# Kernel optimization log

Hardware: AMD Instinct MI355X
Metric: run time of the kernel (lower is better)

Reference implementation:

```python
import jax, jax.numpy as jnp
import numpy as np

N_LAYERS, H, D, DH = 4, 16, 1024, 64
V_FR, V_EN = 32000, 32000
L_FR, L_EN, B = 513, 512, 2


def _pos_enc(x):
    # x: [L, B, D]; pe[i,j] = sin(i/10000^(j/D)) if j even else cos(i/10000^((j-1)/D))
    L, _, D_ = x.shape
    pos = jnp.arange(L, dtype=jnp.float32)[:, None]
    j = jnp.arange(D_)
    ang = pos / jnp.power(10000.0, (j - (j % 2)).astype(jnp.float32) / D_)
    pe = jnp.where(j % 2 == 0, jnp.sin(ang), jnp.cos(ang))
    return x + pe[:, None, :]


def _ln(x, g, b):
    mu = jnp.mean(x, -1, keepdims=True)
    var = jnp.mean((x - mu) ** 2, -1, keepdims=True)
    return (x - mu) * jax.lax.rsqrt(var + 1e-5) * g + b


def _mha(q_in, k_in, v_in, w, bias, causal):
    # w: [3, H, D, dh], bias: [3, H, dh]
    dh = w.shape[-1]
    Q = jnp.einsum('bld,hde->bhle', q_in, w[0]) + bias[0][None, :, None, :]
    K = jnp.einsum('bmd,hde->bhme', k_in, w[1]) + bias[1][None, :, None, :]
    V = jnp.einsum('bmd,hde->bhme', v_in, w[2]) + bias[2][None, :, None, :]
    s = jnp.einsum('bhle,bhme->bhlm', Q, K) / jnp.sqrt(jnp.float32(dh))
    if causal:
        m = jnp.tril(jnp.ones((s.shape[-2], s.shape[-1]), bool))
        s = jnp.where(m, s, -jnp.inf)
    a = jax.nn.softmax(s, axis=-1)
    o = jnp.einsum('bhlm,bhme->bhle', a, V)
    b_, h_, l_, dh_ = o.shape
    return o.transpose(0, 2, 1, 3).reshape(b_, l_, h_ * dh_)


def setup_inputs() -> dict:
    key = jax.random.key(0)
    ks = jax.random.split(key, 24)
    s = 0.02
    rn = lambda k, shp: jax.random.normal(k, shp, jnp.float32) * s
    return {
        'fr': jax.random.randint(ks[0], (L_FR, B), 0, V_FR),
        'en': jax.random.randint(ks[1], (L_EN, B), 0, V_EN),
        'emb_fr': rn(ks[2], (V_FR, D)),
        'emb_en': rn(ks[3], (V_EN, D)),
        'enc_qkv_w': rn(ks[4], (N_LAYERS, 3, H, D, DH)),
        'enc_qkv_b': rn(ks[5], (N_LAYERS, 3, H, DH)),
        'enc_fc1_w': rn(ks[6], (N_LAYERS, D, D)),
        'enc_fc1_b': rn(ks[7], (N_LAYERS, D)),
        'enc_fc2_w': rn(ks[8], (N_LAYERS, D, D)),
        'enc_fc2_b': rn(ks[9], (N_LAYERS, D)),
        'enc_ln_g': jnp.ones((N_LAYERS, 2, D)) + rn(ks[10], (N_LAYERS, 2, D)),
        'enc_ln_b': rn(ks[11], (N_LAYERS, 2, D)),
        'dec_self_qkv_w': rn(ks[12], (N_LAYERS, 3, H, D, DH)),
        'dec_self_qkv_b': rn(ks[13], (N_LAYERS, 3, H, DH)),
        'dec_cross_qkv_w': rn(ks[14], (N_LAYERS, 3, H, D, DH)),
        'dec_cross_qkv_b': rn(ks[15], (N_LAYERS, 3, H, DH)),
        'dec_fc1_w': rn(ks[16], (N_LAYERS, D, D)),
        'dec_fc1_b': rn(ks[17], (N_LAYERS, D)),
        'dec_fc2_w': rn(ks[18], (N_LAYERS, D, D)),
        'dec_fc2_b': rn(ks[19], (N_LAYERS, D)),
        'dec_ln_g': jnp.ones((N_LAYERS, 3, D)) + rn(ks[20], (N_LAYERS, 3, D)),
        'dec_ln_b': rn(ks[21], (N_LAYERS, 3, D)),
        'out_w': rn(ks[22], (D, V_EN)),
        'out_b': rn(ks[23], (V_EN,)),
    }


def reference(fr, en, emb_fr, emb_en, enc_qkv_w, enc_qkv_b, enc_fc1_w, enc_fc1_b,
              enc_fc2_w, enc_fc2_b, enc_ln_g, enc_ln_b, dec_self_qkv_w,
              dec_self_qkv_b, dec_cross_qkv_w, dec_cross_qkv_b, dec_fc1_w,
              dec_fc1_b, dec_fc2_w, dec_fc2_b, dec_ln_g, dec_ln_b, out_w, out_b):
    # Encoder (dropout p=0 -> identity in eval math)
    x = _pos_enc(emb_fr[fr[1:]]).transpose(1, 0, 2)  # [B, L_src, D]
    for n in range(N_LAYERS):
        a = _mha(x, x, x, enc_qkv_w[n], enc_qkv_b[n], causal=False)
        x = _ln(x + a, enc_ln_g[n, 0], enc_ln_b[n, 0])
        h = jnp.maximum(x @ enc_fc1_w[n] + enc_fc1_b[n], 0.0) @ enc_fc2_w[n] + enc_fc2_b[n]
        x = _ln(x + h, enc_ln_g[n, 1], enc_ln_b[n, 1])
    enc_out = x
    # Decoder
    y = _pos_enc(emb_en[en]).transpose(1, 0, 2)  # [B, L_tgt, D]
    for n in range(N_LAYERS):
        a = _mha(y, y, y, dec_self_qkv_w[n], dec_self_qkv_b[n], causal=True)
        y = _ln(y + a, dec_ln_g[n, 0], dec_ln_b[n, 0])
        c = _mha(y, enc_out, enc_out, dec_cross_qkv_w[n], dec_cross_qkv_b[n], causal=False)
        y = _ln(y + c, dec_ln_g[n, 1], dec_ln_b[n, 1])
        h = jnp.maximum(y @ dec_fc1_w[n] + dec_fc1_b[n], 0.0) @ dec_fc2_w[n] + dec_fc2_b[n]
        y = _ln(y + h, dec_ln_g[n, 2], dec_ln_b[n, 2])
    return y @ out_w + out_b  # [B, L_tgt, V_EN]
```

## Files before the change

kernel.cpp:

```cpp
#include <hip/hip_runtime.h>
#include <stdint.h>
#include <stddef.h>

typedef unsigned short u16;
typedef __attribute__((ext_vector_type(8))) short bf16x8;
typedef __attribute__((ext_vector_type(4))) float f32x4;

#define DEV __device__ __forceinline__

DEV float b2f(u16 u) { union { float f; uint32_t i; } v; v.i = ((uint32_t)u) << 16; return v.f; }
DEV u16 f2b(float f) {
  uint32_t x = __float_as_uint(f);
  x += 0x7fffu + ((x >> 16) & 1u);
  return (u16)(x >> 16);
}
DEV bf16x8 ld8f(const float* f) {
  float4 a = *(const float4*)f;
  float4 b = *(const float4*)(f + 4);
  bf16x8 r;
  ((u16*)&r)[0] = f2b(a.x); ((u16*)&r)[1] = f2b(a.y);
  ((u16*)&r)[2] = f2b(a.z); ((u16*)&r)[3] = f2b(a.w);
  ((u16*)&r)[4] = f2b(b.x); ((u16*)&r)[5] = f2b(b.y);
  ((u16*)&r)[6] = f2b(b.z); ((u16*)&r)[7] = f2b(b.w);
  return r;
}
DEV void gload16(const u16* g, u16* l) {
  __builtin_amdgcn_global_load_lds((const __attribute__((address_space(1))) void*)g,
                                   (__attribute__((address_space(3))) void*)l, 16, 0, 0);
}
DEV f32x4 mfma16(bf16x8 a, bf16x8 b, f32x4 c) {
  return __builtin_amdgcn_mfma_f32_16x16x32_bf16(a, b, c, 0, 0, 0);
}

__global__ __launch_bounds__(256) void transpose_w(const float* __restrict__ src,
                                                   u16* __restrict__ dst, int K, int N) {
  __shared__ u16 t[32][33];
  int tx = threadIdx.x, ty = threadIdx.y;
  int k0 = blockIdx.x * 32, n0 = blockIdx.y * 32;
  size_t base = (size_t)blockIdx.z * K * N;
#pragma unroll
  for (int i = 0; i < 4; i++) {
    int k = ty + 8 * i;
    t[k][tx] = f2b(src[base + (size_t)(k0 + k) * N + n0 + tx]);
  }
  __syncthreads();
#pragma unroll
  for (int i = 0; i < 4; i++) {
    int n = ty + 8 * i;
    dst[base + (size_t)(n0 + n) * K + k0 + tx] = t[tx][n];
  }
}

__global__ __launch_bounds__(256) void embed_k(const int* __restrict__ tok, const float* __restrict__ emb,
                                               float* __restrict__ o32, u16* __restrict__ ob, int shift) {
  int row = blockIdx.x;
  int b = row >> 9, l = row & 511;
  int tk = tok[(size_t)(l + shift) * 2 + b];
  const float* e = emb + (size_t)tk * 1024;
  const float c0 = -9.210340371976184f / 1024.f;
#pragma unroll
  for (int i = 0; i < 4; i++) {
    int d = threadIdx.x + i * 256;
    int j2 = d & ~1;
    float ang = (float)l * expf(c0 * (float)j2);
    float pe = (d & 1) ? cosf(ang) : sinf(ang);
    float rv = e[d] + pe;
    o32[(size_t)row * 1024 + d] = rv;
    ob[(size_t)row * 1024 + d] = f2b(rv);
  }
}

__global__ __launch_bounds__(256) void ln_k(const float* a, const float* d,
                                            const float* __restrict__ g, const float* __restrict__ bb,
                                            float* o32, u16* __restrict__ ob) {
  int row = blockIdx.x;
  int tid = threadIdx.x;
  const float4 av = ((const float4*)(a + (size_t)row * 1024))[tid];
  const float4 dv = ((const float4*)(d + (size_t)row * 1024))[tid];
  float v[4] = {av.x + dv.x, av.y + dv.y, av.z + dv.z, av.w + dv.w};
  float s = 0.f, s2 = 0.f;
#pragma unroll
  for (int i = 0; i < 4; i++) { s += v[i]; s2 += v[i] * v[i]; }
#pragma unroll
  for (int off = 1; off < 64; off <<= 1) {
    s += __shfl_xor(s, off);
    s2 += __shfl_xor(s2, off);
  }
  __shared__ float red[8];
  int wid = tid >> 6;
  if ((tid & 63) == 0) { red[wid * 2] = s; red[wid * 2 + 1] = s2; }
  __syncthreads();
  s = red[0] + red[2] + red[4] + red[6];
  s2 = red[1] + red[3] + red[5] + red[7];
  float mu = s * (1.f / 1024.f);
  float var = s2 * (1.f / 1024.f) - mu * mu;
  float inv = rsqrtf(var + 1e-5f);
  const float4 gv = ((const float4*)g)[tid];
  const float4 bv = ((const float4*)bb)[tid];
  float4 ov;
  ov.x = (v[0] - mu) * inv * gv.x + bv.x;
  ov.y = (v[1] - mu) * inv * gv.y + bv.y;
  ov.z = (v[2] - mu) * inv * gv.z + bv.z;
  ov.w = (v[3] - mu) * inv * gv.w + bv.w;
  ((float4*)(o32 + (size_t)row * 1024))[tid] = ov;
  uint2 p;
  p.x = (uint32_t)f2b(ov.x) | ((uint32_t)f2b(ov.y) << 16);
  p.y = (uint32_t)f2b(ov.z) | ((uint32_t)f2b(ov.w) << 16);
  ((uint2*)(ob + (size_t)row * 1024))[tid] = p;
}

template <int BM, int BN, bool RELU, bool OUT32>
__global__ __launch_bounds__(256) void gemm_tile(const u16* __restrict__ A, const u16* __restrict__ BT,
                                                 const float* __restrict__ bias, void* __restrict__ out,
                                                 int N, int K) {
  constexpr int FM = BM / 32, FN = BN / 32;
  __shared__ __align__(16) u16 lA[BM * 32];
  __shared__ __align__(16) u16 lB[BN * 32];
  int bx = blockIdx.x, by = blockIdx.y;
  int tid = threadIdx.x, lane = tid & 63, wid = tid >> 6;
  int l15 = lane & 15, lg = lane >> 4;
  int bm = by * BM, bn = bx * BN;
  int wr = (wid >> 1) * (BM / 2), wc = (wid & 1) * (BN / 2);
  f32x4 acc[FM][FN] = {};
  int r_s = tid >> 2, c_s = tid & 3;
  for (int kt = 0; kt < K; kt += 32) {
    __syncthreads();
#pragma unroll
    for (int i = 0; i < BM / 64; i++)
      gload16(A + (size_t)(bm + i * 64 + r_s) * K + kt + c_s * 8, &lA[(size_t)(i * 256 + wid * 64) * 8]);
#pragma unroll
    for (int i = 0; i < BN / 64; i++)
      gload16(BT + (size_t)(bn + i * 64 + r_s) * K + kt + c_s * 8, &lB[(size_t)(i * 256 + wid * 64) * 8]);
    __syncthreads();
    bf16x8 af[FM], bf_[FN];
#pragma unroll
    for (int m = 0; m < FM; m++) af[m] = *(const bf16x8*)&lA[(wr + m * 16 + l15) * 32 + lg * 8];
#pragma unroll
    for (int n = 0; n < FN; n++) bf_[n] = *(const bf16x8*)&lB[(wc + n * 16 + l15) * 32 + lg * 8];
#pragma unroll
    for (int m = 0; m < FM; m++)
#pragma unroll
      for (int n = 0; n < FN; n++) acc[m][n] = mfma16(af[m], bf_[n], acc[m][n]);
  }
#pragma unroll
  for (int n = 0; n < FN; n++) {
    int col = bn + wc + n * 16 + l15;
    float bv = bias[col];
#pragma unroll
    for (int m = 0; m < FM; m++) {
#pragma unroll
      for (int r = 0; r < 4; r++) {
        int row = bm + wr + m * 16 + lg * 4 + r;
        float v = acc[m][n][r] + bv;
        if (RELU) v = fmaxf(v, 0.f);
        if (OUT32) ((float*)out)[(size_t)row * N + col] = v;
        else ((u16*)out)[(size_t)row * N + col] = f2b(v);
      }
    }
  }
}

template <int BM, int BN>
__global__ __launch_bounds__(256) void gemm_p3(const u16* __restrict__ A, const u16* __restrict__ BT,
                                               const float* __restrict__ bias, float* __restrict__ out,
                                               int N, int K) {
  constexpr int FM = BM / 32, FN = BN / 32;
  constexpr int L = BM / 64 + BN / 64;
  __shared__ __align__(16) u16 lA[3][BM * 32];
  __shared__ __align__(16) u16 lB[3][BN * 32];
  int b = blockIdx.x;
  int p = (b & 7) + 8 * (b >> 6);
  if (p >= N / BN) return;
  int bx = p, by = (b >> 3) & 7;
  int tid = threadIdx.x, lane = tid & 63, wid = tid >> 6;
  int l15 = lane & 15, lg = lane >> 4;
  int bm = by * BM, bn = bx * BN;
  int wr = (wid >> 1) * (BM / 2), wc = (wid & 1) * (BN / 2);
  f32x4 acc[FM][FN] = {};
  int r_s = tid >> 2, c_s = tid & 3;
  auto stage = [&](int buf, int kt) {
#pragma unroll
    for (int i = 0; i < BM / 64; i++)
      gload16(A + (size_t)(bm + i * 64 + r_s) * K + kt + c_s * 8, &lA[buf][(i * 256 + wid * 64) * 8]);
#pragma unroll
    for (int i = 0; i < BN / 64; i++)
      gload16(BT + (size_t)(bn + i * 64 + r_s) * K + kt + c_s * 8, &lB[buf][(i * 256 + wid * 64) * 8]);
  };
  int nt = K >> 5;
  stage(0, 0);
  stage(1, 32);
  asm volatile("s_waitcnt vmcnt(%0)" ::"n"(L) : "memory");
  __builtin_amdgcn_s_barrier();
  int cur = 0;
  for (int t = 0; t < nt; t++) {
    if (t + 2 < nt) stage(cur == 0 ? 2 : cur - 1, (t + 2) * 32);
    bf16x8 af[FM], bf_[FN];
#pragma unroll
    for (int m = 0; m < FM; m++) af[m] = *(const bf16x8*)&lA[cur][(wr + m * 16 + l15) * 32 + lg * 8];
#pragma unroll
    for (int n = 0; n < FN; n++) bf_[n] = *(const bf16x8*)&lB[cur][(wc + n * 16 + l15) * 32 + lg * 8];
#pragma unroll
    for (int m = 0; m < FM; m++)
#pragma unroll
      for (int n = 0; n < FN; n++) acc[m][n] = mfma16(af[m], bf_[n], acc[m][n]);
    if (t + 2 < nt) {
      asm volatile("s_waitcnt vmcnt(%0)" ::"n"(L) : "memory");
    } else if (t + 1 < nt) {
      asm volatile("s_waitcnt vmcnt(0)" ::: "memory");
    }
    if (t + 1 < nt) __builtin_amdgcn_s_barrier();
    cur = (cur == 2) ? 0 : cur + 1;
  }
#pragma unroll
  for (int n = 0; n < FN; n++) {
    int col = bn + wc + n * 16 + l15;
    float bv = bias[col];
#pragma unroll
    for (int m = 0; m < FM; m++) {
#pragma unroll
      for (int r = 0; r < 4; r++) {
        int row = bm + wr + m * 16 + lg * 4 + r;
        out[(size_t)row * N + col] = acc[m][n][r] + bv;
      }
    }
  }
}

__global__ __launch_bounds__(256) void gemm_qkv2(const u16* __restrict__ Aq, const u16* __restrict__ Akv,
                                                 const u16* __restrict__ WT, const float* __restrict__ bias,
                                                 u16* __restrict__ Qo, u16* __restrict__ Ko,
                                                 u16* __restrict__ Vto) {
  __shared__ __align__(16) u16 lA[64 * 32];
  __shared__ __align__(16) u16 lB[64 * 32];
  int bx = blockIdx.x, by = blockIdx.y;
  int t = bx >> 4;
  const u16* A = (t == 0) ? Aq : Akv;
  int tid = threadIdx.x, lane = tid & 63, wid = tid >> 6;
  int l15 = lane & 15, lg = lane >> 4;
  int bm = by * 64, bn = bx * 64;
  int wr = (wid >> 1) * 32, wc = (wid & 1) * 32;
  f32x4 acc[2][2] = {};
  int r_s = tid >> 2, c_s = tid & 3;
  for (int kt = 0; kt < 1024; kt += 32) {
    __syncthreads();
    gload16(A + (size_t)(bm + r_s) * 1024 + kt + c_s * 8, &lA[(size_t)(wid * 64) * 8]);
    gload16(WT + (size_t)(bn + r_s) * 1024 + kt + c_s * 8, &lB[(size_t)(wid * 64) * 8]);
    __syncthreads();
    bf16x8 af[2], bf_[2];
#pragma unroll
    for (int m = 0; m < 2; m++) af[m] = *(const bf16x8*)&lA[(wr + m * 16 + l15) * 32 + lg * 8];
#pragma unroll
    for (int n = 0; n < 2; n++) bf_[n] = *(const bf16x8*)&lB[(wc + n * 16 + l15) * 32 + lg * 8];
#pragma unroll
    for (int m = 0; m < 2; m++)
#pragma unroll
      for (int n = 0; n < 2; n++) acc[m][n] = mfma16(af[m], bf_[n], acc[m][n]);
  }
#pragma unroll
  for (int n = 0; n < 2; n++) {
    int col = bn + wc + n * 16 + l15;
    int h = (col >> 6) & 15, e = col & 63;
    float bv = bias[col];
#pragma unroll
    for (int m = 0; m < 2; m++) {
#pragma unroll
      for (int r = 0; r < 4; r++) {
        int row = bm + wr + m * 16 + lg * 4 + r;
        int b = row >> 9, l = row & 511;
        u16 vbv = f2b(acc[m][n][r] + bv);
        size_t bhead = (size_t)b * 16 + h;
        if (t == 0) Qo[(bhead * 512 + l) * 64 + e] = vbv;
        else if (t == 1) Ko[(bhead * 512 + l) * 64 + e] = vbv;
        else Vto[(bhead * 64 + e) * 512 + l] = vbv;
      }
    }
  }
}

__global__ __launch_bounds__(256) void gemm_bn(const u16* __restrict__ A, const float* __restrict__ B,
                                               const float* __restrict__ bias, float* __restrict__ out,
                                               int N, int K) {
  __shared__ __align__(16) u16 lA[128 * 32];
  __shared__ __align__(16) u16 lBn[32 * 128];
  int b = blockIdx.x;
  int p = (b & 7) + 8 * (b >> 6);
  if (p >= N / 128) return;
  int by = (b >> 3) & 7;
  int tid = threadIdx.x, lane = tid & 63;
  int wid = tid >> 6;
  int l15 = lane & 15, lg = lane >> 4;
  int bm = by * 128, bn = p * 128;
  int wr = (wid >> 1) * 64, wc = (wid & 1) * 64;
  f32x4 acc[4][4] = {};
  int r_s = tid >> 2, c_s = tid & 3;
  int br = tid >> 4, bc = tid & 15;
  for (int kt = 0; kt < K; kt += 32) {
    bf16x8 va[2], vb[2];
#pragma unroll
    for (int it = 0; it < 2; it++) {
      va[it] = *(const bf16x8*)&A[(size_t)(bm + it * 64 + r_s) * K + kt + c_s * 8];
      vb[it] = ld8f(B + (size_t)(kt + it * 16 + br) * N + bn + bc * 8);
    }
    __syncthreads();
#pragma unroll
    for (int it = 0; it < 2; it++) {
      *(bf16x8*)&lA[(size_t)(it * 256 + tid) * 8] = va[it];
      *(bf16x8*)&lBn[(size_t)(it * 256 + tid) * 8] = vb[it];
    }
    __syncthreads();
    bf16x8 af[4], bfr[4];
#pragma unroll
    for (int m = 0; m < 4; m++) af[m] = *(const bf16x8*)&lA[(wr + m * 16 + l15) * 32 + lg * 8];
#pragma unroll
    for (int n = 0; n < 4; n++) {
#pragma unroll
      for (int j = 0; j < 8; j++)
        ((short*)&bfr[n])[j] = (short)lBn[(lg * 8 + j) * 128 + wc + n * 16 + l15];
    }
#pragma unroll
    for (int m = 0; m < 4; m++)
#pragma unroll
      for (int n = 0; n < 4; n++) acc[m][n] = mfma16(af[m], bfr[n], acc[m][n]);
  }
#pragma unroll
  for (int n = 0; n < 4; n++) {
    int col = bn + wc + n * 16 + l15;
    float bv = bias[col];
#pragma unroll
    for (int m = 0; m < 4; m++) {
#pragma unroll
      for (int r = 0; r < 4; r++) {
        int row = bm + wr + m * 16 + lg * 4 + r;
        out[(size_t)row * N + col] = acc[m][n][r] + bv;
      }
    }
  }
}

template <bool CAUSAL>
__global__ __launch_bounds__(256) void attn_k(const u16* __restrict__ Qb, const u16* __restrict__ Kb,
                                              const u16* __restrict__ Vtb, float* __restrict__ Ob) {
  int bh = blockIdx.y;
  int tid = threadIdx.x, lane = tid & 63, w = tid >> 6;
  int l15 = lane & 15, lg = lane >> 4;
  int q0 = blockIdx.x * 64 + w * 16;
  const u16* Qh = Qb + (size_t)bh * 512 * 64;
  const u16* Kh = Kb + (size_t)bh * 512 * 64;
  const u16* Vh = Vtb + (size_t)bh * 64 * 512;
  __shared__ __align__(16) u16 P[4][16 * 40];
  u16* Pw = &P[w][0];
  bf16x8 qa0 = *(const bf16x8*)&Qh[(size_t)(q0 + l15) * 64 + lg * 8];
  bf16x8 qa1 = *(const bf16x8*)&Qh[(size_t)(q0 + l15) * 64 + 32 + lg * 8];
  f32x4 acc[4];
#pragma unroll
  for (int c = 0; c < 4; c++) acc[c] = (f32x4){0.f, 0.f, 0.f, 0.f};
  float ls[4] = {0.f, 0.f, 0.f, 0.f};
  int ktend = CAUSAL ? ((q0 + 15) >> 5) : 15;
  for (int kt = 0; kt <= ktend; kt++) {
    int kv = kt * 32;
    f32x4 z = (f32x4){0.f, 0.f, 0.f, 0.f};
    bf16x8 k00 = *(const bf16x8*)&Kh[(size_t)(kv + l15) * 64 + lg * 8];
    bf16x8 k01 = *(const bf16x8*)&Kh[(size_t)(kv + l15) * 64 + 32 + lg * 8];
    f32x4 s0 = mfma16(qa0, k00, z);
    s0 = mfma16(qa1, k01, s0);
    bf16x8 k10 = *(const bf16x8*)&Kh[(size_t)(kv + 16 + l15) * 64 + lg * 8];
    bf16x8 k11 = *(const bf16x8*)&Kh[(size_t)(kv + 16 + l15) * 64 + 32 + lg * 8];
    f32x4 s1 = mfma16(qa0, k10, z);
    s1 = mfma16(qa1, k11, s1);
#pragma unroll
    for (int r = 0; r < 4; r++) {
      float a0 = s0[r] * 0.125f, a1 = s1[r] * 0.125f;
      if (CAUSAL) {
        int rowg = q0 + lg * 4 + r;
        if (kv + l15 > rowg) a0 = -1e30f;
        if (kv + 16 + l15 > rowg) a1 = -1e30f;
      }
      float p0 = __expf(a0), p1 = __expf(a1);
      ls[r] += p0 + p1;
      int prow = lg * 4 + r;
      Pw[prow * 40 + l15] = f2b(p0);
      Pw[prow * 40 + 16 + l15] = f2b(p1);
    }
    bf16x8 pa = *(const bf16x8*)&Pw[l15 * 40 + lg * 8];
#pragma unroll
    for (int c = 0; c < 4; c++) {
      bf16x8 vb = *(const bf16x8*)&Vh[(size_t)(c * 16 + l15) * 512 + kv + lg * 8];
      acc[c] = mfma16(pa, vb, acc[c]);
    }
  }
#pragma unroll
  for (int r = 0; r < 4; r++) {
#pragma unroll
    for (int off = 1; off < 16; off <<= 1) ls[r] += __shfl_xor(ls[r], off);
  }
  int b = bh >> 4, h = bh & 15;
#pragma unroll
  for (int r = 0; r < 4; r++) {
    float inv = 1.f / ls[r];
    int rowg = q0 + lg * 4 + r;
    float* orow = Ob + (size_t)(b * 512 + rowg) * 1024 + h * 64;
#pragma unroll
    for (int c = 0; c < 4; c++) orow[c * 16 + l15] = acc[c][r] * inv;
  }
}

extern "C" void kernel_launch(void* const* d_in, const int* in_sizes, int n_in,
                              void* d_out, int out_size, void* d_ws, size_t ws_size,
                              hipStream_t stream) {
  const int* fr = (const int*)d_in[0];
  const int* en = (const int*)d_in[1];
  const float* emb_fr = (const float*)d_in[2];
  const float* emb_en = (const float*)d_in[3];
  const float* enc_qkv_w = (const float*)d_in[4];
  const float* enc_qkv_b = (const float*)d_in[5];
  const float* enc_fc1_w = (const float*)d_in[6];
  const float* enc_fc1_b = (const float*)d_in[7];
  const float* enc_fc2_w = (const float*)d_in[8];
  const float* enc_fc2_b = (const float*)d_in[9];
  const float* enc_ln_g = (const float*)d_in[10];
  const float* enc_ln_bb = (const float*)d_in[11];
  const float* dec_self_qkv_w = (const float*)d_in[12];
  const float* dec_self_qkv_b = (const float*)d_in[13];
  const float* dec_cross_qkv_w = (const float*)d_in[14];
  const float* dec_cross_qkv_b = (const float*)d_in[15];
  const float* dec_fc1_w = (const float*)d_in[16];
  const float* dec_fc1_b = (const float*)d_in[17];
  const float* dec_fc2_w = (const float*)d_in[18];
  const float* dec_fc2_b = (const float*)d_in[19];
  const float* dec_ln_g = (const float*)d_in[20];
  const float* dec_ln_bb = (const float*)d_in[21];
  const float* out_w = (const float*)d_in[22];
  const float* out_b = (const float*)d_in[23];

  char* o8 = (char*)d_out;
  u16* qkvT_d = (u16*)o8;
  u16* fcT_d = (u16*)(o8 + 6291456);
  float* x32 = (float*)(o8 + 8388608);
  float* y32 = (float*)(o8 + 12582912);
  float* d32 = (float*)(o8 + 16777216);
  u16* xb = (u16*)(o8 + 20971520);
  u16* hb = (u16*)(o8 + 23068672);
  u16* Qb = (u16*)(o8 + 25165824);
  u16* Kb = (u16*)(o8 + 27262976);
  u16* Vtb = (u16*)(o8 + 29360128);

  char* w8 = (char*)d_ws;
  u16* yb = (u16*)w8;
  u16* outwT = (u16*)(w8 + 2097152);
  u16* eqkvT = (u16*)(w8 + 67633152);
  u16* dsqkvT = (u16*)(w8 + 92798976);
  u16* dcqkvT = (u16*)(w8 + 117964800);
  u16* efc1T = (u16*)(w8 + 143130624);
  u16* efc2T = (u16*)(w8 + 151519232);
  u16* dfc1T = (u16*)(w8 + 159907840);
  u16* dfc2T = (u16*)(w8 + 168296448);
  int tier = (ws_size >= 176685056u) ? 2 : (ws_size >= 67633152u) ? 1 : 0;

  dim3 tb(32, 8);
  if (tier >= 1)
    transpose_w<<<dim3(32, 1000, 1), tb, 0, stream>>>(out_w, outwT, 1024, 32000);
  if (tier == 2) {
    transpose_w<<<dim3(32, 2, 192), tb, 0, stream>>>(enc_qkv_w, eqkvT, 1024, 64);
    transpose_w<<<dim3(32, 2, 192), tb, 0, stream>>>(dec_self_qkv_w, dsqkvT, 1024, 64);
    transpose_w<<<dim3(32, 2, 192), tb, 0, stream>>>(dec_cross_qkv_w, dcqkvT, 1024, 64);
    transpose_w<<<dim3(32, 32, 4), tb, 0, stream>>>(enc_fc1_w, efc1T, 1024, 1024);
    transpose_w<<<dim3(32, 32, 4), tb, 0, stream>>>(enc_fc2_w, efc2T, 1024, 1024);
    transpose_w<<<dim3(32, 32, 4), tb, 0, stream>>>(dec_fc1_w, dfc1T, 1024, 1024);
    transpose_w<<<dim3(32, 32, 4), tb, 0, stream>>>(dec_fc2_w, dfc2T, 1024, 1024);
  }

  embed_k<<<1024, 256, 0, stream>>>(fr, emb_fr, x32, xb, 1);
  embed_k<<<1024, 256, 0, stream>>>(en, emb_en, y32, yb, 0);

  for (int n = 0; n < 4; n++) {
    const u16* wqkv;
    if (tier == 2) wqkv = eqkvT + (size_t)n * 3145728;
    else {
      transpose_w<<<dim3(32, 2, 48), tb, 0, stream>>>(enc_qkv_w + (size_t)n * 48 * 65536, qkvT_d, 1024, 64);
      wqkv = qkvT_d;
    }
    gemm_qkv2<<<dim3(48, 16), 256, 0, stream>>>(xb, xb, wqkv, enc_qkv_b + (size_t)n * 3072, Qb, Kb, Vtb);
    attn_k<false><<<dim3(8, 32), 256, 0, stream>>>(Qb, Kb, Vtb, d32);
    ln_k<<<1024, 256, 0, stream>>>(x32, d32, enc_ln_g + (size_t)(n * 2) * 1024,
                                   enc_ln_bb + (size_t)(n * 2) * 1024, x32, xb);
    const u16* w1;
    if (tier == 2) w1 = efc1T + (size_t)n * 1048576;
    else {
      transpose_w<<<dim3(32, 32, 1), tb, 0, stream>>>(enc_fc1_w + (size_t)n * 1048576, fcT_d, 1024, 1024);
      w1 = fcT_d;
    }
    gemm_tile<64, 64, true, false><<<dim3(16, 16), 256, 0, stream>>>(
        xb, w1, enc_fc1_b + (size_t)n * 1024, hb, 1024, 1024);
    const u16* w2;
    if (tier == 2) w2 = efc2T + (size_t)n * 1048576;
    else {
      transpose_w<<<dim3(32, 32, 1), tb, 0, stream>>>(enc_fc2_w + (size_t)n * 1048576, fcT_d, 1024, 1024);
      w2 = fcT_d;
    }
    gemm_tile<64, 64, false, true><<<dim3(16, 16), 256, 0, stream>>>(
        hb, w2, enc_fc2_b + (size_t)n * 1024, d32, 1024, 1024);
    ln_k<<<1024, 256, 0, stream>>>(x32, d32, enc_ln_g + (size_t)(n * 2 + 1) * 1024,
                                   enc_ln_bb + (size_t)(n * 2 + 1) * 1024, x32, xb);
  }
  for (int n = 0; n < 4; n++) {
    const u16* wq;
    if (tier == 2) wq = dsqkvT + (size_t)n * 3145728;
    else {
      transpose_w<<<dim3(32, 2, 48), tb, 0, stream>>>(dec_self_qkv_w + (size_t)n * 48 * 65536, qkvT_d, 1024, 64);
      wq = qkvT_d;
    }
    gemm_qkv2<<<dim3(48, 16), 256, 0, stream>>>(yb, yb, wq, dec_self_qkv_b + (size_t)n * 3072, Qb, Kb, Vtb);
    attn_k<true><<<dim3(8, 32), 256, 0, stream>>>(Qb, Kb, Vtb, d32);
    ln_k<<<1024, 256, 0, stream>>>(y32, d32, dec_ln_g + (size_t)(n * 3) * 1024,
                                   dec_ln_bb + (size_t)(n * 3) * 1024, y32, yb);
    if (tier == 2) wq = dcqkvT + (size_t)n * 3145728;
    else {
      transpose_w<<<dim3(32, 2, 48), tb, 0, stream>>>(dec_cross_qkv_w + (size_t)n * 48 * 65536, qkvT_d, 1024, 64);
      wq = qkvT_d;
    }
    gemm_qkv2<<<dim3(48, 16), 256, 0, stream>>>(yb, xb, wq, dec_cross_qkv_b + (size_t)n * 3072, Qb, Kb, Vtb);
    attn_k<false><<<dim3(8, 32), 256, 0, stream>>>(Qb, Kb, Vtb, d32);
    ln_k<<<1024, 256, 0, stream>>>(y32, d32, dec_ln_g + (size_t)(n * 3 + 1) * 1024,
                                   dec_ln_bb + (size_t)(n * 3 + 1) * 1024, y32, yb);
    const u16* w1;
    if (tier == 2) w1 = dfc1T + (size_t)n * 1048576;
    else {
      transpose_w<<<dim3(32, 32, 1), tb, 0, stream>>>(dec_fc1_w + (size_t)n * 1048576, fcT_d, 1024, 1024);
      w1 = fcT_d;
    }
    gemm_tile<64, 64, true, false><<<dim3(16, 16), 256, 0, stream>>>(
        yb, w1, dec_fc1_b + (size_t)n * 1024, hb, 1024, 1024);
    const u16* w2;
    if (tier == 2) w2 = dfc2T + (size_t)n * 1048576;
    else {
      transpose_w<<<dim3(32, 32, 1), tb, 0, stream>>>(dec_fc2_w + (size_t)n * 1048576, fcT_d, 1024, 1024);
      w2 = fcT_d;
    }
    gemm_tile<64, 64, false, true><<<dim3(16, 16), 256, 0, stream>>>(
        hb, w2, dec_fc2_b + (size_t)n * 1024, d32, 1024, 1024);
    ln_k<<<1024, 256, 0, stream>>>(y32, d32, dec_ln_g + (size_t)(n * 3 + 2) * 1024,
                                   dec_ln_bb + (size_t)(n * 3 + 2) * 1024, y32, yb);
  }
  if (tier >= 1)
    gemm_p3<128, 128><<<dim3(2048), 256, 0, stream>>>(yb, outwT, out_b, (float*)d_out, 32000, 1024);
  else
    gemm_bn<<<dim3(2048), 256, 0, stream>>>(yb, out_w, out_b, (float*)d_out, 32000, 1024);
}
```

Before: 1.030 ms.

## Split attention KV loop across wave pairs and shrink output GEMM tile

The attention kernel now gives each 16-query tile to two waves. Each wave processes alternate 32-key chunks, and the partial accumulators and row sums are combined through shared memory before normalisation. This doubles the attention grid to raise occupancy, since only 256 blocks ran before. The vocab-projection GEMM also moves from 128x128 to 64x128 tiles with a parameterised block swizzle and twice as many blocks. The smaller tile trades operand reuse for finer scheduling granularity, and the attention change adds an LDS round trip and a block-wide barrier.

```diff
diff --git a/kernel.cpp b/kernel.cpp
--- a/kernel.cpp
+++ b/kernel.cpp
@@ -160,7 +160,7 @@
   }
 }
 
-template <int BM, int BN>
+template <int BM, int BN, int RS, int RM>
 __global__ __launch_bounds__(256) void gemm_p3(const u16* __restrict__ A, const u16* __restrict__ BT,
                                                const float* __restrict__ bias, float* __restrict__ out,
                                                int N, int K) {
@@ -169,9 +169,9 @@
   __shared__ __align__(16) u16 lA[3][BM * 32];
   __shared__ __align__(16) u16 lB[3][BN * 32];
   int b = blockIdx.x;
-  int p = (b & 7) + 8 * (b >> 6);
+  int p = (b & 7) + 8 * (b >> RS);
   if (p >= N / BN) return;
-  int bx = p, by = (b >> 3) & 7;
+  int bx = p, by = (b >> 3) & RM;
   int tid = threadIdx.x, lane = tid & 63, wid = tid >> 6;
   int l15 = lane & 15, lg = lane >> 4;
   int bm = by * BM, bn = bx * BN;
@@ -342,12 +342,14 @@
                                               const u16* __restrict__ Vtb, float* __restrict__ Ob) {
   int bh = blockIdx.y;
   int tid = threadIdx.x, lane = tid & 63, w = tid >> 6;
+  int qh = w >> 1, kh = w & 1;
   int l15 = lane & 15, lg = lane >> 4;
-  int q0 = blockIdx.x * 64 + w * 16;
+  int q0 = blockIdx.x * 32 + qh * 16;
   const u16* Qh = Qb + (size_t)bh * 512 * 64;
   const u16* Kh = Kb + (size_t)bh * 512 * 64;
   const u16* Vh = Vtb + (size_t)bh * 64 * 512;
   __shared__ __align__(16) u16 P[4][16 * 40];
+  __shared__ float CMB[2][64][21];
   u16* Pw = &P[w][0];
   bf16x8 qa0 = *(const bf16x8*)&Qh[(size_t)(q0 + l15) * 64 + lg * 8];
   bf16x8 qa1 = *(const bf16x8*)&Qh[(size_t)(q0 + l15) * 64 + 32 + lg * 8];
@@ -356,7 +358,7 @@
   for (int c = 0; c < 4; c++) acc[c] = (f32x4){0.f, 0.f, 0.f, 0.f};
   float ls[4] = {0.f, 0.f, 0.f, 0.f};
   int ktend = CAUSAL ? ((q0 + 15) >> 5) : 15;
-  for (int kt = 0; kt <= ktend; kt++) {
+  for (int kt = kh; kt <= ktend; kt += 2) {
     int kv = kt * 32;
     f32x4 z = (f32x4){0.f, 0.f, 0.f, 0.f};
     bf16x8 k00 = *(const bf16x8*)&Kh[(size_t)(kv + l15) * 64 + lg * 8];
@@ -388,19 +390,35 @@
       acc[c] = mfma16(pa, vb, acc[c]);
     }
   }
-#pragma unroll
-  for (int r = 0; r < 4; r++) {
-#pragma unroll
-    for (int off = 1; off < 16; off <<= 1) ls[r] += __shfl_xor(ls[r], off);
-  }
-  int b = bh >> 4, h = bh & 15;
-#pragma unroll
-  for (int r = 0; r < 4; r++) {
-    float inv = 1.f / ls[r];
-    int rowg = q0 + lg * 4 + r;
-    float* orow = Ob + (size_t)(b * 512 + rowg) * 1024 + h * 64;
-#pragma unroll
-    for (int c = 0; c < 4; c++) orow[c * 16 + l15] = acc[c][r] * inv;
+  if (kh == 1) {
+#pragma unroll
+    for (int c = 0; c < 4; c++)
+#pragma unroll
+      for (int r = 0; r < 4; r++) CMB[qh][lane][c * 4 + r] = acc[c][r];
+#pragma unroll
+    for (int r = 0; r < 4; r++) CMB[qh][lane][16 + r] = ls[r];
+  }
+  __syncthreads();
+  if (kh == 0) {
+#pragma unroll
+    for (int c = 0; c < 4; c++)
+#pragma unroll
+      for (int r = 0; r < 4; r++) acc[c][r] += CMB[qh][lane][c * 4 + r];
+#pragma unroll
+    for (int r = 0; r < 4; r++) {
+      ls[r] += CMB[qh][lane][16 + r];
+#pragma unroll
+      for (int off = 1; off < 16; off <<= 1) ls[r] += __shfl_xor(ls[r], off);
+    }
+    int b = bh >> 4, h = bh & 15;
+#pragma unroll
+    for (int r = 0; r < 4; r++) {
+      float inv = 1.f / ls[r];
+      int rowg = q0 + lg * 4 + r;
+      float* orow = Ob + (size_t)(b * 512 + rowg) * 1024 + h * 64;
+#pragma unroll
+      for (int c = 0; c < 4; c++) orow[c * 16 + l15] = acc[c][r] * inv;
+    }
   }
 }
 
@@ -480,7 +498,7 @@
       wqkv = qkvT_d;
     }
     gemm_qkv2<<<dim3(48, 16), 256, 0, stream>>>(xb, xb, wqkv, enc_qkv_b + (size_t)n * 3072, Qb, Kb, Vtb);
-    attn_k<false><<<dim3(8, 32), 256, 0, stream>>>(Qb, Kb, Vtb, d32);
+    attn_k<false><<<dim3(16, 32), 256, 0, stream>>>(Qb, Kb, Vtb, d32);
     ln_k<<<1024, 256, 0, stream>>>(x32, d32, enc_ln_g + (size_t)(n * 2) * 1024,
                                    enc_ln_bb + (size_t)(n * 2) * 1024, x32, xb);
     const u16* w1;
@@ -510,7 +528,7 @@
       wq = qkvT_d;
     }
     gemm_qkv2<<<dim3(48, 16), 256, 0, stream>>>(yb, yb, wq, dec_self_qkv_b + (size_t)n * 3072, Qb, Kb, Vtb);
-    attn_k<true><<<dim3(8, 32), 256, 0, stream>>>(Qb, Kb, Vtb, d32);
+    attn_k<true><<<dim3(16, 32), 256, 0, stream>>>(Qb, Kb, Vtb, d32);
     ln_k<<<1024, 256, 0, stream>>>(y32, d32, dec_ln_g + (size_t)(n * 3) * 1024,
                                    dec_ln_bb + (size_t)(n * 3) * 1024, y32, yb);
     if (tier == 2) wq = dcqkvT + (size_t)n * 3145728;
@@ -519,7 +537,7 @@
       wq = qkvT_d;
     }
     gemm_qkv2<<<dim3(48, 16), 256, 0, stream>>>(yb, xb, wq, dec_cross_qkv_b + (size_t)n * 3072, Qb, Kb, Vtb);
-    attn_k<false><<<dim3(8, 32), 256, 0, stream>>>(Qb, Kb, Vtb, d32);
+    attn_k<false><<<dim3(16, 32), 256, 0, stream>>>(Qb, Kb, Vtb, d32);
     ln_k<<<1024, 256, 0, stream>>>(y32, d32, dec_ln_g + (size_t)(n * 3 + 1) * 1024,
                                    dec_ln_bb + (size_t)(n * 3 + 1) * 1024, y32, yb);
     const u16* w1;
@@ -542,7 +560,7 @@
                                    dec_ln_bb + (size_t)(n * 3 + 2) * 1024, y32, yb);
   }
   if (tier >= 1)
-    gemm_p3<128, 128><<<dim3(2048), 256, 0, stream>>>(yb, outwT, out_b, (float*)d_out, 32000, 1024);
+    gemm_p3<64, 128, 7, 15><<<dim3(4096), 256, 0, stream>>>(yb, outwT, out_b, (float*)d_out, 32000, 1024);
   else
     gemm_bn<<<dim3(2048), 256, 0, stream>>>(yb, out_w, out_b, (float*)d_out, 32000, 1024);
 }
```

New measurement: 1.048 ms. Within noise of the previous version (+1.8%).
